# Kernel tuning notes

Measured on AMD Instinct MI355X. Metric: run time of the kernel, lower is better.

## Reference

```python
import jax, jax.numpy as jnp
import numpy as np

B, C, W, H = 8, 256, 64, 64
CQ = C // 8  # f/g projection dim


def setup_inputs() -> dict:
    key = jax.random.key(0)
    ks = jax.random.split(key, 8)
    x = jax.random.normal(ks[0], (B, C, W, H), dtype=jnp.float32)
    y = jax.random.normal(ks[1], (B, C, W, H), dtype=jnp.float32)
    # 1x1 conv weights stored as [out, in] matrices (xavier-uniform-like scale)
    def xavier(k, o, i):
        lim = float(np.sqrt(6.0 / (o + i)))
        return jax.random.uniform(k, (o, i), dtype=jnp.float32, minval=-lim, maxval=lim)
    Wf = xavier(ks[2], CQ, C); bf = jnp.zeros((CQ,), jnp.float32)
    Wg = xavier(ks[3], CQ, C); bg = jnp.zeros((CQ,), jnp.float32)
    Wh = xavier(ks[4], C, C);  bh = jnp.zeros((C,), jnp.float32)
    gamma = jnp.zeros((1,), jnp.float32)
    return {"x": x, "y": y, "Wf": Wf, "bf": bf, "Wg": Wg, "bg": bg,
            "Wh": Wh, "bh": bh, "gamma": gamma}


def reference(x, y, Wf, bf, Wg, bg, Wh, bh, gamma):
    b, c, w, h = x.shape
    n = w * h
    xf = x.reshape(b, c, n)  # [B,C,N]
    yf = y.reshape(b, c, n)
    f = jnp.einsum('dc,bcn->bdn', Wf, xf) + bf[None, :, None]  # [B,CQ,N]
    g = jnp.einsum('dc,bcn->bdn', Wg, yf) + bg[None, :, None]  # [B,CQ,N]
    hh = jnp.einsum('dc,bcn->bdn', Wh, xf) + bh[None, :, None]  # [B,C,N]
    # attention[b,i,j] = sum_d f[b,d,i] * g[b,d,j]; softmax over j (no 1/sqrt(d) scaling)
    attn = jax.nn.softmax(jnp.einsum('bdi,bdj->bij', f, g), axis=-1)  # [B,N,N]
    sa = jnp.einsum('bcn,bin->bci', hh, attn.transpose(0, 2, 1))  # h @ attn: [B,C,N]
    sa = jnp.einsum('bcj,bij->bci', hh, attn)  # equivalent, clean: sum_j h[:, :, j]*attn[:, i, j]
    out = gamma[0] * sa.reshape(b, c, w, h) + x
    return out
```

## Files before the change

kernel.cpp:

```cpp
#include <hip/hip_runtime.h>
#include <math.h>

#define BB      8
#define C_DIM   256
#define NN      4096
#define CQ_DIM  32
#define LOG2E   1.44269504088896f

typedef __bf16 bf16_t;
typedef bf16_t bf16x4 __attribute__((ext_vector_type(4)));
typedef bf16_t bf16x8 __attribute__((ext_vector_type(8)));
typedef float  f32x16 __attribute__((ext_vector_type(16)));

#if defined(__has_builtin)
#if __has_builtin(__builtin_amdgcn_exp2f)
#define EXP2F(x) __builtin_amdgcn_exp2f(x)
#else
#define EXP2F(x) exp2f(x)
#endif
#else
#define EXP2F(x) exp2f(x)
#endif

#define MFMA32(a, b, c) __builtin_amdgcn_mfma_f32_32x32x16_bf16((a), (b), (c), 0, 0, 0)

__device__ __forceinline__ void gload_lds16(const bf16_t* g, bf16_t* l)
{
    __builtin_amdgcn_global_load_lds(
        (const __attribute__((address_space(1))) void*)g,
        (__attribute__((address_space(3))) void*)l, 16, 0, 0);
}

__global__ __launch_bounds__(256) void cast_weights(
    const float* __restrict__ Wh, const float* __restrict__ Wf,
    const float* __restrict__ Wg, bf16_t* __restrict__ Whp,
    bf16_t* __restrict__ Wfp, bf16_t* __restrict__ Wgp)
{
    const int id = blockIdx.x * 256 + threadIdx.x;
    if (id < 65536) {
        const int e = id & 7, lane = (id >> 3) & 63;
        const int s = (id >> 9) & 15, m = id >> 13;
        const int l31 = lane & 31, half = lane >> 5;
        Whp[id] = (bf16_t)Wh[(m * 32 + l31) * 256 + s * 16 + half * 8 + e];
    } else if (id < 73728) {
        const int q = id - 65536;
        const int e = q & 7, lane = (q >> 3) & 63, s = q >> 9;
        const int l31 = lane & 31, half = lane >> 5;
        Wfp[q] = (bf16_t)Wf[l31 * 256 + s * 16 + half * 8 + e];
    } else if (id < 81920) {
        const int q = id - 73728;
        const int e = q & 7, lane = (q >> 3) & 63, s = q >> 9;
        const int l31 = lane & 31, half = lane >> 5;
        Wgp[q] = (bf16_t)Wg[l31 * 256 + s * 16 + half * 8 + e];
    }
}

__global__ __launch_bounds__(256) void prep_fused(
    const float* __restrict__ x, const float* __restrict__ y,
    const bf16_t* __restrict__ Whp, const bf16_t* __restrict__ Wfp,
    const bf16_t* __restrict__ Wgp,
    const float* __restrict__ bh, const float* __restrict__ bfv,
    const float* __restrict__ bg,
    bf16_t* __restrict__ Qw, bf16_t* __restrict__ Kw, bf16_t* __restrict__ Vw)
{
    const int id   = blockIdx.x;
    const bool isx = id < 512;
    const int bid  = id & 511;
    const int b    = bid & 7;
    const int n0   = (bid >> 3) * 64;
    const float* src = isx ? x : y;

    __shared__ float ftile[64][65];
    __shared__ __align__(16) bf16_t Xb[64 * 256];

    const int t = threadIdx.x;
    const int w = t >> 6, lane = t & 63, l31 = lane & 31, half = lane >> 5;
    const int col = t & 63, rbase = t >> 6;

    for (int cs = 0; cs < 4; ++cs) {
        if (cs) __syncthreads();
#pragma unroll
        for (int rr = 0; rr < 16; ++rr) {
            const int crow = rbase + 4 * rr;
            ftile[col][crow] =
                src[((size_t)b * C_DIM + cs * 64 + crow) * NN + n0 + col];
        }
        __syncthreads();
#pragma unroll
        for (int p = 0; p < 2; ++p) {
            const int chunk = t + p * 256;
            const int nl = chunk >> 3, ck = chunk & 7;
            bf16x8 v;
#pragma unroll
            for (int j = 0; j < 8; ++j) v[j] = (bf16_t)ftile[nl][ck * 8 + j];
            const int slot = (cs * 8 + ck) ^ (nl & 15);
            *(bf16x8*)&Xb[nl * 256 + slot * 8] = v;
        }
    }
    __syncthreads();

    auto xbfrag = [&](int nloc, int s) -> bf16x8 {
        return *(const bf16x8*)&Xb[nloc * 256 +
                                   (((s * 2 + half) ^ (nloc & 15)) << 3)];
    };

    if (w < 2) {
        const int nloc = w * 32 + l31;
        const bf16_t* Wp = (isx ? Wfp : Wgp) + lane * 8;
        const float*  bp = isx ? bfv : bg;
        f32x16 acc = {};
        for (int s = 0; s < 16; ++s) {
            const bf16x8 af = *(const bf16x8*)(Wp + s * 512);
            acc = MFMA32(af, xbfrag(nloc, s), acc);
        }
        bf16_t* dst = (isx ? Qw : Kw) + ((size_t)b * NN + n0 + nloc) * CQ_DIM;
#pragma unroll
        for (int rq = 0; rq < 4; ++rq) {
            const int d0 = 8 * rq + 4 * half;
            bf16x4 v4;
#pragma unroll
            for (int ri = 0; ri < 4; ++ri)
                v4[ri] = (bf16_t)(acc[4 * rq + ri] + bp[d0 + ri]);
            *(bf16x4*)(dst + d0) = v4;
        }
    }

    if (isx) {
#pragma unroll
        for (int mi = 0; mi < 2; ++mi) {
            const int m = 2 * w + mi;
            const bf16_t* Ap = Whp + (size_t)m * 8192 + lane * 8;
            f32x16 a0 = {}, a1 = {};
            for (int s = 0; s < 16; ++s) {
                const bf16x8 af = *(const bf16x8*)(Ap + s * 512);
                a0 = MFMA32(af, xbfrag(l31, s), a0);
                a1 = MFMA32(af, xbfrag(32 + l31, s), a1);
            }
#pragma unroll
            for (int r = 0; r < 16; ++r) {
                const int co = m * 32 + (r & 3) + 8 * (r >> 2) + 4 * half;
                const float bb = bh[co];
                bf16_t* vp = Vw + ((size_t)b * C_DIM + co) * NN + n0 + l31;
                vp[0]  = (bf16_t)(a0[r] + bb);
                vp[32] = (bf16_t)(a1[r] + bb);
            }
        }
    }
}

__global__ __launch_bounds__(512, 2) void attn_fused(
    const bf16_t* __restrict__ Q, const bf16_t* __restrict__ K,
    const bf16_t* __restrict__ V, const float* __restrict__ x,
    const float* __restrict__ gamma, float* __restrict__ out)
{
    const int id = blockIdx.x;
    const int b  = id & 7;
    const int i0 = (id >> 3) * 64;
    const int t  = threadIdx.x;
    const int w = t >> 6, lane = t & 63, l31 = lane & 31, half = lane >> 5;
    const int qg = w >> 2;
    const int jg = w & 3;
    const int cbx = ((jg & 1) << 2) | (jg & 2);

    __shared__ __align__(16) bf16_t Vlds[2][256 * 128];
    __shared__ float lpart[4 * 64];
    __shared__ float linv_s[64];

    const int r8h = 8 * half;

    const bf16_t* Qp = Q + ((size_t)(b * NN + i0 + qg * 32 + l31)) * CQ_DIM + r8h;
    const bf16x8 qf0 = *(const bf16x8*)Qp;
    const bf16x8 qf1 = *(const bf16x8*)(Qp + 16);

    const int pj = (l31 & 19) | ((l31 & 4) << 1) | ((l31 & 8) >> 1);
    const bf16_t* Kcur = K + ((size_t)b * NN + jg * 32 + pj) * CQ_DIM + r8h;

    const int sa = lane & 15, sb = lane >> 4;
    const bf16_t* Vrow0 = V + ((size_t)b * C_DIM + w * 32 + sb) * NN;
    int joff[8];
#pragma unroll
    for (int i = 0; i < 8; ++i)
        joff[i] = 8 * (sa ^ ((i * 4 + sb) & 15));

    const int vsw  = l31 & 15;
    const int vrow = l31 * 128;
    const int p0 = (((jg * 4) + half) ^ vsw) << 3;
    const int p1 = (((jg * 4) + 2 + half) ^ vsw) << 3;

    float lacc = 0.f;
    f32x16 O[8] = {{}, {}, {}, {}, {}, {}, {}, {}};
    bf16x8 frag[2];

    bf16_t* vcur = &Vlds[0][0];
    bf16_t* vnxt = &Vlds[1][0];

    auto do_stage = [&](int j0e, bf16_t* vb) {
        bf16_t* d = vb + w * 4096;
#pragma unroll
        for (int i = 0; i < 8; ++i)
            gload_lds16(Vrow0 + (size_t)(i * 4) * NN + j0e + joff[i],
                        d + i * 512);
    };

    auto do_S = [&](const bf16x8 kf0, const bf16x8 kf1) {
        f32x16 s = {};
        s = MFMA32(kf0, qf0, s);
        s = MFMA32(kf1, qf1, s);
        bf16x8 q0, q1;
#pragma unroll
        for (int r = 0; r < 8; ++r) {
            const float pv = EXP2F(s[r] * LOG2E);
            lacc += pv; q0[r] = (bf16_t)pv;
        }
#pragma unroll
        for (int r = 8; r < 16; ++r) {
            const float pv = EXP2F(s[r] * LOG2E);
            lacc += pv; q1[r - 8] = (bf16_t)pv;
        }
        frag[0] = q0;
        frag[1] = q1;
    };

    auto do_PV = [&](const bf16_t* vb) {
#pragma unroll
        for (int i = 0; i < 8; ++i) {
            const int rb = ((i ^ cbx) << 12) + vrow;
            const bf16x8 v0 = *(const bf16x8*)&vb[rb + p0];
            const bf16x8 v1 = *(const bf16x8*)&vb[rb + p1];
            O[i] = MFMA32(frag[0], v0, O[i]);
            O[i] = MFMA32(frag[1], v1, O[i]);
        }
    };

    {
        const bf16x8 k0 = *(const bf16x8*)Kcur;
        const bf16x8 k1 = *(const bf16x8*)(Kcur + 16);
        Kcur += 128 * CQ_DIM;
        do_stage(0, vcur);
        do_S(k0, k1);
    }
    __syncthreads();

    for (int tt = 0; tt < 31; ++tt) {
        const bf16x8 k0 = *(const bf16x8*)Kcur;
        const bf16x8 k1 = *(const bf16x8*)(Kcur + 16);
        Kcur += 128 * CQ_DIM;
        do_stage((tt + 1) * 128, vnxt);
        do_PV(vcur);
        do_S(k0, k1);
        __syncthreads();
        bf16_t* tmp = vcur; vcur = vnxt; vnxt = tmp;
    }
    do_PV(vcur);

    lacc += __shfl_xor(lacc, 32, 64);
    if (half == 0) lpart[jg * 64 + qg * 32 + l31] = lacc;
    __syncthreads();
    if (t < 64)
        linv_s[t] = 1.0f / (lpart[t] + lpart[64 + t] + lpart[128 + t] + lpart[192 + t]);

    float* red = (float*)&Vlds[0][0];
    const int qsw = l31 & 7;
    const int myA = w * 4096;

    {
        float* s = red + myA;
#pragma unroll
        for (int k = 0; k < 4; ++k)
#pragma unroll
            for (int r4 = 0; r4 < 4; ++r4) {
                const int quad = 2 * r4 + half;
                float4 v4 = { O[4 + k][4 * r4 + 0], O[4 + k][4 * r4 + 1],
                              O[4 + k][4 * r4 + 2], O[4 + k][4 * r4 + 3] };
                *(float4*)&s[k * 1024 + l31 * 32 + ((quad ^ qsw) << 2)] = v4;
            }
    }
    __syncthreads();
    {
        const float* s = red + (w ^ 1) * 4096;
#pragma unroll
        for (int k = 0; k < 4; ++k)
#pragma unroll
            for (int r4 = 0; r4 < 4; ++r4) {
                const int quad = 2 * r4 + half;
                const float4 v4 = *(const float4*)&s[k * 1024 + l31 * 32 + ((quad ^ qsw) << 2)];
                O[k][4 * r4 + 0] += v4.x;
                O[k][4 * r4 + 1] += v4.y;
                O[k][4 * r4 + 2] += v4.z;
                O[k][4 * r4 + 3] += v4.w;
            }
    }
    __syncthreads();
    {
        float* s = red + myA;
#pragma unroll
        for (int k = 0; k < 2; ++k)
#pragma unroll
            for (int r4 = 0; r4 < 4; ++r4) {
                const int quad = 2 * r4 + half;
                float4 v4 = { O[2 + k][4 * r4 + 0], O[2 + k][4 * r4 + 1],
                              O[2 + k][4 * r4 + 2], O[2 + k][4 * r4 + 3] };
                *(float4*)&s[k * 1024 + l31 * 32 + ((quad ^ qsw) << 2)] = v4;
            }
    }
    __syncthreads();
    {
        const float* s = red + (w ^ 2) * 4096;
#pragma unroll
        for (int k = 0; k < 2; ++k)
#pragma unroll
            for (int r4 = 0; r4 < 4; ++r4) {
                const int quad = 2 * r4 + half;
                const float4 v4 = *(const float4*)&s[k * 1024 + l31 * 32 + ((quad ^ qsw) << 2)];
                O[k][4 * r4 + 0] += v4.x;
                O[k][4 * r4 + 1] += v4.y;
                O[k][4 * r4 + 2] += v4.z;
                O[k][4 * r4 + 3] += v4.w;
            }
    }

    const float g = gamma[0];
#pragma unroll
    for (int k = 0; k < 2; ++k) {
        const int ch = (k ^ cbx) * 32 + l31;
        const size_t base = ((size_t)b * C_DIM + ch) * NN + i0 + qg * 32 + 4 * half;
#pragma unroll
        for (int r4 = 0; r4 < 4; ++r4) {
            const size_t idx = base + 8 * r4;
            const int rb = qg * 32 + 8 * r4 + 4 * half;
            const float4 xv = *(const float4*)(x + idx);
            float4 o;
            o.x = fmaf(g, O[k][4 * r4 + 0] * linv_s[rb + 0], xv.x);
            o.y = fmaf(g, O[k][4 * r4 + 1] * linv_s[rb + 1], xv.y);
            o.z = fmaf(g, O[k][4 * r4 + 2] * linv_s[rb + 2], xv.z);
            o.w = fmaf(g, O[k][4 * r4 + 3] * linv_s[rb + 3], xv.w);
            *(float4*)(out + idx) = o;
        }
    }
}

extern "C" void kernel_launch(void* const* d_in, const int* in_sizes, int n_in,
                              void* d_out, int out_size, void* d_ws, size_t ws_size,
                              hipStream_t stream)
{
    const float* x     = (const float*)d_in[0];
    const float* y     = (const float*)d_in[1];
    const float* Wf    = (const float*)d_in[2];
    const float* bf    = (const float*)d_in[3];
    const float* Wg    = (const float*)d_in[4];
    const float* bg    = (const float*)d_in[5];
    const float* Wh    = (const float*)d_in[6];
    const float* bh    = (const float*)d_in[7];
    const float* gamma = (const float*)d_in[8];
    float* out = (float*)d_out;

    bf16_t* bufA = (bf16_t*)d_ws;
    bf16_t* Qw   = bufA + (size_t)BB * NN * C_DIM;
    bf16_t* Kw   = Qw + (size_t)BB * NN * CQ_DIM;
    bf16_t* Whp  = Kw + (size_t)BB * NN * CQ_DIM;
    bf16_t* Wfp  = Whp + C_DIM * C_DIM;
    bf16_t* Wgp  = Wfp + CQ_DIM * C_DIM;

    cast_weights<<<320, 256, 0, stream>>>(Wh, Wf, Wg, Whp, Wfp, Wgp);
    prep_fused<<<1024, 256, 0, stream>>>(x, y, Whp, Wfp, Wgp,
                                         bh, bf, bg, Qw, Kw, bufA);
    attn_fused<<<BB * (NN / 64), 512, 0, stream>>>(Qw, Kw, bufA, x, gamma, out);
}
```

Before: 225.9 us.

## Merge x/y projection blocks and prioritize MFMA waves in attention loop

```diff
diff --git a/kernel.cpp b/kernel.cpp
--- a/kernel.cpp
+++ b/kernel.cpp
@@ -63,87 +63,108 @@
     const float* __restrict__ bg,
     bf16_t* __restrict__ Qw, bf16_t* __restrict__ Kw, bf16_t* __restrict__ Vw)
 {
-    const int id   = blockIdx.x;
-    const bool isx = id < 512;
-    const int bid  = id & 511;
-    const int b    = bid & 7;
-    const int n0   = (bid >> 3) * 64;
-    const float* src = isx ? x : y;
-
-    __shared__ float ftile[64][65];
+    const int id = blockIdx.x;
+    const int b  = id & 7;
+    const int n0 = (id >> 3) * 64;
+
     __shared__ __align__(16) bf16_t Xb[64 * 256];
+    __shared__ __align__(16) bf16_t Yb[64 * 256];
 
     const int t = threadIdx.x;
     const int w = t >> 6, lane = t & 63, l31 = lane & 31, half = lane >> 5;
-    const int col = t & 63, rbase = t >> 6;
-
-    for (int cs = 0; cs < 4; ++cs) {
-        if (cs) __syncthreads();
-#pragma unroll
-        for (int rr = 0; rr < 16; ++rr) {
-            const int crow = rbase + 4 * rr;
-            ftile[col][crow] =
-                src[((size_t)b * C_DIM + cs * 64 + crow) * NN + n0 + col];
-        }
-        __syncthreads();
-#pragma unroll
-        for (int p = 0; p < 2; ++p) {
-            const int chunk = t + p * 256;
-            const int nl = chunk >> 3, ck = chunk & 7;
-            bf16x8 v;
-#pragma unroll
-            for (int j = 0; j < 8; ++j) v[j] = (bf16_t)ftile[nl][ck * 8 + j];
-            const int slot = (cs * 8 + ck) ^ (nl & 15);
-            *(bf16x8*)&Xb[nl * 256 + slot * 8] = v;
-        }
-    }
-    __syncthreads();
-
-    auto xbfrag = [&](int nloc, int s) -> bf16x8 {
-        return *(const bf16x8*)&Xb[nloc * 256 +
-                                   (((s * 2 + half) ^ (nloc & 15)) << 3)];
+
+    const int crow0 = w * 2 + (lane >> 5);
+    const int nA = (lane & 31) * 2, nB = nA + 1;
+    const size_t off0 = ((size_t)b * C_DIM + crow0) * NN + n0 + nA;
+
+    float2 xv[32];
+#pragma unroll
+    for (int i = 0; i < 32; ++i)
+        xv[i] = *(const float2*)(x + off0 + (size_t)(i * 8) * NN);
+
+#pragma unroll
+    for (int i = 0; i < 32; ++i) {
+        Xb[nA * 256 + ((i ^ (nA & 15)) << 3) + crow0] = (bf16_t)xv[i].x;
+        Xb[nB * 256 + ((i ^ (nB & 15)) << 3) + crow0] = (bf16_t)xv[i].y;
+    }
+
+    float2 yv[32];
+#pragma unroll
+    for (int i = 0; i < 32; ++i)
+        yv[i] = *(const float2*)(y + off0 + (size_t)(i * 8) * NN);
+    asm volatile("" ::: "memory");
+
+    __syncthreads();
+
+    auto bfrag = [&](const bf16_t* buf, int nloc, int s) -> bf16x8 {
+        return *(const bf16x8*)&buf[nloc * 256 +
+                                    (((s * 2 + half) ^ (nloc & 15)) << 3)];
     };
 
     if (w < 2) {
         const int nloc = w * 32 + l31;
-        const bf16_t* Wp = (isx ? Wfp : Wgp) + lane * 8;
-        const float*  bp = isx ? bfv : bg;
+        const bf16_t* Wp = Wfp + lane * 8;
         f32x16 acc = {};
         for (int s = 0; s < 16; ++s) {
             const bf16x8 af = *(const bf16x8*)(Wp + s * 512);
-            acc = MFMA32(af, xbfrag(nloc, s), acc);
-        }
-        bf16_t* dst = (isx ? Qw : Kw) + ((size_t)b * NN + n0 + nloc) * CQ_DIM;
+            acc = MFMA32(af, bfrag(Xb, nloc, s), acc);
+        }
+        bf16_t* dst = Qw + ((size_t)b * NN + n0 + nloc) * CQ_DIM;
 #pragma unroll
         for (int rq = 0; rq < 4; ++rq) {
             const int d0 = 8 * rq + 4 * half;
             bf16x4 v4;
 #pragma unroll
             for (int ri = 0; ri < 4; ++ri)
-                v4[ri] = (bf16_t)(acc[4 * rq + ri] + bp[d0 + ri]);
+                v4[ri] = (bf16_t)(acc[4 * rq + ri] + bfv[d0 + ri]);
             *(bf16x4*)(dst + d0) = v4;
         }
     }
 
-    if (isx) {
-#pragma unroll
-        for (int mi = 0; mi < 2; ++mi) {
-            const int m = 2 * w + mi;
-            const bf16_t* Ap = Whp + (size_t)m * 8192 + lane * 8;
-            f32x16 a0 = {}, a1 = {};
-            for (int s = 0; s < 16; ++s) {
-                const bf16x8 af = *(const bf16x8*)(Ap + s * 512);
-                a0 = MFMA32(af, xbfrag(l31, s), a0);
-                a1 = MFMA32(af, xbfrag(32 + l31, s), a1);
-            }
-#pragma unroll
-            for (int r = 0; r < 16; ++r) {
-                const int co = m * 32 + (r & 3) + 8 * (r >> 2) + 4 * half;
-                const float bb = bh[co];
-                bf16_t* vp = Vw + ((size_t)b * C_DIM + co) * NN + n0 + l31;
-                vp[0]  = (bf16_t)(a0[r] + bb);
-                vp[32] = (bf16_t)(a1[r] + bb);
-            }
+#pragma unroll
+    for (int mi = 0; mi < 2; ++mi) {
+        const int m = 2 * w + mi;
+        const bf16_t* Ap = Whp + (size_t)m * 8192 + lane * 8;
+        f32x16 a0 = {}, a1 = {};
+        for (int s = 0; s < 16; ++s) {
+            const bf16x8 af = *(const bf16x8*)(Ap + s * 512);
+            a0 = MFMA32(af, bfrag(Xb, l31, s), a0);
+            a1 = MFMA32(af, bfrag(Xb, 32 + l31, s), a1);
+        }
+#pragma unroll
+        for (int r = 0; r < 16; ++r) {
+            const int co = m * 32 + (r & 3) + 8 * (r >> 2) + 4 * half;
+            const float bb = bh[co];
+            bf16_t* vp = Vw + ((size_t)b * C_DIM + co) * NN + n0 + l31;
+            vp[0]  = (bf16_t)(a0[r] + bb);
+            vp[32] = (bf16_t)(a1[r] + bb);
+        }
+    }
+
+#pragma unroll
+    for (int i = 0; i < 32; ++i) {
+        Yb[nA * 256 + ((i ^ (nA & 15)) << 3) + crow0] = (bf16_t)yv[i].x;
+        Yb[nB * 256 + ((i ^ (nB & 15)) << 3) + crow0] = (bf16_t)yv[i].y;
+    }
+    __syncthreads();
+
+    if (w < 2) {
+        const int nloc = w * 32 + l31;
+        const bf16_t* Wp = Wgp + lane * 8;
+        f32x16 acc = {};
+        for (int s = 0; s < 16; ++s) {
+            const bf16x8 af = *(const bf16x8*)(Wp + s * 512);
+            acc = MFMA32(af, bfrag(Yb, nloc, s), acc);
+        }
+        bf16_t* dst = Kw + ((size_t)b * NN + n0 + nloc) * CQ_DIM;
+#pragma unroll
+        for (int rq = 0; rq < 4; ++rq) {
+            const int d0 = 8 * rq + 4 * half;
+            bf16x4 v4;
+#pragma unroll
+            for (int ri = 0; ri < 4; ++ri)
+                v4[ri] = (bf16_t)(acc[4 * rq + ri] + bg[d0 + ri]);
+            *(bf16x4*)(dst + d0) = v4;
         }
     }
 }
@@ -202,19 +223,16 @@
                         d + i * 512);
     };
 
-    auto do_S = [&](const bf16x8 kf0, const bf16x8 kf1) {
-        f32x16 s = {};
-        s = MFMA32(kf0, qf0, s);
-        s = MFMA32(kf1, qf1, s);
+    auto do_exp = [&](const f32x16& sv) {
         bf16x8 q0, q1;
 #pragma unroll
         for (int r = 0; r < 8; ++r) {
-            const float pv = EXP2F(s[r] * LOG2E);
+            const float pv = EXP2F(sv[r] * LOG2E);
             lacc += pv; q0[r] = (bf16_t)pv;
         }
 #pragma unroll
         for (int r = 8; r < 16; ++r) {
-            const float pv = EXP2F(s[r] * LOG2E);
+            const float pv = EXP2F(sv[r] * LOG2E);
             lacc += pv; q1[r - 8] = (bf16_t)pv;
         }
         frag[0] = q0;
@@ -237,7 +255,10 @@
         const bf16x8 k1 = *(const bf16x8*)(Kcur + 16);
         Kcur += 128 * CQ_DIM;
         do_stage(0, vcur);
-        do_S(k0, k1);
+        f32x16 sv = {};
+        sv = MFMA32(k0, qf0, sv);
+        sv = MFMA32(k1, qf1, sv);
+        do_exp(sv);
     }
     __syncthreads();
 
@@ -246,12 +267,19 @@
         const bf16x8 k1 = *(const bf16x8*)(Kcur + 16);
         Kcur += 128 * CQ_DIM;
         do_stage((tt + 1) * 128, vnxt);
+        __builtin_amdgcn_s_setprio(1);
         do_PV(vcur);
-        do_S(k0, k1);
+        f32x16 sv = {};
+        sv = MFMA32(k0, qf0, sv);
+        sv = MFMA32(k1, qf1, sv);
+        __builtin_amdgcn_s_setprio(0);
+        do_exp(sv);
         __syncthreads();
         bf16_t* tmp = vcur; vcur = vnxt; vnxt = tmp;
     }
+    __builtin_amdgcn_s_setprio(1);
     do_PV(vcur);
+    __builtin_amdgcn_s_setprio(0);
 
     lacc += __shfl_xor(lacc, 32, 64);
     if (half == 0) lpart[jg * 64 + qg * 32 + l31] = lacc;
@@ -362,7 +390,7 @@
     bf16_t* Wgp  = Wfp + CQ_DIM * C_DIM;
 
     cast_weights<<<320, 256, 0, stream>>>(Wh, Wf, Wg, Whp, Wfp, Wgp);
-    prep_fused<<<1024, 256, 0, stream>>>(x, y, Whp, Wfp, Wgp,
-                                         bh, bf, bg, Qw, Kw, bufA);
+    prep_fused<<<512, 256, 0, stream>>>(x, y, Whp, Wfp, Wgp,
+                                        bh, bf, bg, Qw, Kw, bufA);
     attn_fused<<<BB * (NN / 64), 512, 0, stream>>>(Qw, Kw, bufA, x, gamma, out);
 }
```

Result: no change. 227.6 us (+0.7%).
